# Kernel tuning notes

Measured on AMD Instinct MI355X. Metric: run time of the kernel, lower is better.

Reference implementation:

```python
import jax, jax.numpy as jnp
import numpy as np

NCLASS = 21  # num_classes from init
EPS = 1e-6


def setup_inputs() -> dict:
    key = jax.random.key(0)
    k1, k2 = jax.random.split(key)
    feats = jax.random.normal(k1, (8, 256, 64, 64), dtype=jnp.float32)
    masks = jax.random.randint(k2, (8, 256, 256), 0, NCLASS, dtype=jnp.int32)
    return {"feats": feats, "masks": masks}


def reference(feats, masks):
    # feats: [B, C, h, w] float; masks: [B, H, W] int labels
    B, C, _, _ = feats.shape
    H, W = masks.shape[-2:]
    # F.interpolate(..., mode='bilinear', align_corners=False) == half-pixel bilinear resize
    f = jax.image.resize(feats, (B, C, H, W), method="bilinear")  # [B,C,H,W]
    f_flat = f.reshape(B, C, H * W)  # [B,C,P]

    # labels > nclass (e.g. 255 ignore) are clamped to the dump bucket `nclass`;
    # pixels with label == nclass are excluded (one_hot drops out-of-range rows).
    lbl = jnp.where(masks > NCLASS, NCLASS, masks).reshape(B, H * W)  # [B,P]
    onehot = jax.nn.one_hot(lbl, NCLASS, dtype=f.dtype)  # [B,P,K], dump bucket -> all zeros

    # segment-reduce: per-image per-class feature sums and pixel counts
    sums = jnp.einsum("bcp,bpk->bkc", f_flat, onehot)  # [B,K,C]
    counts = onehot.sum(axis=1)  # [B,K]
    per_img = sums / (counts[..., None] + EPS)  # [B,K,C]; absent classes -> ~0, matching torch loop skip
    prototypes = per_img.mean(axis=0)  # [K,C] (sum over batch / b)
    return prototypes
```

## Files before the change

### kernel.cpp

```cpp
#include <hip/hip_runtime.h>

#define NK 21
#define NC 256
#define NSRC 64
#define NOUT 256
#define NB 8
#define NSL 128
#define NG 8
#define EPS 1e-6f

__device__ __forceinline__ void lds_fadd(float* p, float v) {
  __hip_atomic_fetch_add(p, v, __ATOMIC_RELAXED, __HIP_MEMORY_SCOPE_WORKGROUP);
}

__global__ __launch_bounds__(256, 4)
void proto_main(const float* __restrict__ feats,
                const int* __restrict__ masks,
                float* __restrict__ psum,
                float* __restrict__ pcnt) {
  __shared__ __align__(16) float Wl[NK * 32];
  __shared__ int hist[NK];

  const int tid = threadIdx.x;
  const int r0 = blockIdx.x;
  const int b = blockIdx.y;
  const int z = blockIdx.z;

  const float4* fbase = (const float4*)(
      feats + ((size_t)(b * NC + tid) << 12) + (size_t)r0 * 64 + 32 * z);
  const float4 f0 = fbase[0], f1 = fbase[1], f2 = fbase[2], f3 = fbase[3];
  const float4 f4 = fbase[4], f5 = fbase[5], f6 = fbase[6], f7 = fbase[7];

  for (int i = tid; i < NK * 32; i += 256) Wl[i] = 0.f;
  if (tid < NK) hist[tid] = 0;
  __syncthreads();

  int ylo = 4 * r0 - 2; if (ylo < 0) ylo = 0;
  int yhi = 4 * r0 + 5; if (yhi > NOUT - 1) yhi = NOUT - 1;
  const int xlo = z ? 126 : 0;
  const int npix = (yhi - ylo + 1) * 130;
  const int own_lo = 4 * r0;

  for (int i = tid; i < npix; i += 256) {
    const int x = xlo + i % 130;
    const int y = ylo + i / 130;
    const int lbl = masks[((size_t)b * NOUT + y) * NOUT + x];
    if ((unsigned)lbl < NK) {
      const int ry = y >> 2, py = y & 3;
      const int j0y = (py < 2) ? ry - 1 : ry;
      const float fy = (py == 0) ? 0.625f : (py == 1) ? 0.875f
                     : (py == 2) ? 0.125f : 0.375f;
      const int rx = x >> 2, px = x & 3;
      const int j0x = (px < 2) ? rx - 1 : rx;
      const float fx = (px == 0) ? 0.625f : (px == 1) ? 0.875f
                     : (px == 2) ? 0.125f : 0.375f;

      const int cx0 = (j0x < 0) ? 0 : j0x;
      const int cx1 = (j0x + 1 > NSRC - 1) ? NSRC - 1 : j0x + 1;
      const float wx0 = 1.f - fx, wx1 = fx;
      const int ry0 = (j0y < 0) ? 0 : j0y;
      const int ry1 = (j0y + 1 > NSRC - 1) ? NSRC - 1 : j0y + 1;
      const float wy0 = 1.f - fy, wy1 = fy;

      float* Wk = &Wl[lbl * 32];
      if (ry0 == r0) {
        if ((cx0 >> 5) == z) lds_fadd(&Wk[cx0 & 31], wy0 * wx0);
        if ((cx1 >> 5) == z) lds_fadd(&Wk[cx1 & 31], wy0 * wx1);
      }
      if (ry1 == r0) {
        if ((cx0 >> 5) == z) lds_fadd(&Wk[cx0 & 31], wy1 * wx0);
        if ((cx1 >> 5) == z) lds_fadd(&Wk[cx1 & 31], wy1 * wx1);
      }
      if (y >= own_lo && y < own_lo + 4 && (x >> 7) == z)
        atomicAdd(&hist[lbl], 1);
    }
  }
  __syncthreads();

  float acc[NK];
#pragma unroll
  for (int k = 0; k < NK; ++k) acc[k] = 0.f;

  const float4* wb = (const float4*)Wl;
#pragma unroll
  for (int k = 0; k < NK; ++k) {
    const float4 w0 = wb[k * 8 + 0], w1 = wb[k * 8 + 1];
    const float4 w2 = wb[k * 8 + 2], w3 = wb[k * 8 + 3];
    float a = acc[k];
    a = fmaf(f0.x, w0.x, a); a = fmaf(f0.y, w0.y, a);
    a = fmaf(f0.z, w0.z, a); a = fmaf(f0.w, w0.w, a);
    a = fmaf(f1.x, w1.x, a); a = fmaf(f1.y, w1.y, a);
    a = fmaf(f1.z, w1.z, a); a = fmaf(f1.w, w1.w, a);
    a = fmaf(f2.x, w2.x, a); a = fmaf(f2.y, w2.y, a);
    a = fmaf(f2.z, w2.z, a); a = fmaf(f2.w, w2.w, a);
    a = fmaf(f3.x, w3.x, a); a = fmaf(f3.y, w3.y, a);
    a = fmaf(f3.z, w3.z, a); a = fmaf(f3.w, w3.w, a);
    acc[k] = a;
  }
#pragma unroll
  for (int k = 0; k < NK; ++k) {
    const float4 w4 = wb[k * 8 + 4], w5 = wb[k * 8 + 5];
    const float4 w6 = wb[k * 8 + 6], w7 = wb[k * 8 + 7];
    float a = acc[k];
    a = fmaf(f4.x, w4.x, a); a = fmaf(f4.y, w4.y, a);
    a = fmaf(f4.z, w4.z, a); a = fmaf(f4.w, w4.w, a);
    a = fmaf(f5.x, w5.x, a); a = fmaf(f5.y, w5.y, a);
    a = fmaf(f5.z, w5.z, a); a = fmaf(f5.w, w5.w, a);
    a = fmaf(f6.x, w6.x, a); a = fmaf(f6.y, w6.y, a);
    a = fmaf(f6.z, w6.z, a); a = fmaf(f6.w, w6.w, a);
    a = fmaf(f7.x, w7.x, a); a = fmaf(f7.y, w7.y, a);
    a = fmaf(f7.z, w7.z, a); a = fmaf(f7.w, w7.w, a);
    acc[k] = a;
  }

  const int sl = r0 * 2 + z;
  float* dst = psum + ((size_t)(b * NSL + sl) * NK) * NC + tid;
#pragma unroll
  for (int k = 0; k < NK; ++k) dst[k * NC] = acc[k];
  if (tid < NK) pcnt[(size_t)(b * NSL + sl) * NK + tid] = (float)hist[tid];
}

__global__ __launch_bounds__(256)
void proto_finalA(const float* __restrict__ psum,
                  const float* __restrict__ pcnt,
                  float* __restrict__ psum2,
                  float* __restrict__ pcnt2) {
  const int k = blockIdx.x;
  const int b = blockIdx.y;
  const int g = blockIdx.z;
  const int c = threadIdx.x;
  const int sl0 = g * 16;
  float s = 0.f, cnt = 0.f;
#pragma unroll
  for (int j = 0; j < 16; ++j) {
    s += psum[((size_t)(b * NSL + sl0 + j) * NK + k) * NC + c];
    cnt += pcnt[(size_t)(b * NSL + sl0 + j) * NK + k];
  }
  psum2[((size_t)(b * NG + g) * NK + k) * NC + c] = s;
  if (c == 0) pcnt2[(size_t)(b * NG + g) * NK + k] = cnt;
}

__global__ __launch_bounds__(256)
void proto_finalB(const float* __restrict__ psum2,
                  const float* __restrict__ pcnt2,
                  float* __restrict__ out) {
  const int k = blockIdx.x;
  const int c = threadIdx.x;
  float a = 0.f;
#pragma unroll
  for (int b = 0; b < NB; ++b) {
    float s = 0.f, cnt = 0.f;
#pragma unroll
    for (int g = 0; g < NG; ++g) {
      s += psum2[((size_t)(b * NG + g) * NK + k) * NC + c];
      cnt += pcnt2[(size_t)(b * NG + g) * NK + k];
    }
    a += s / (cnt + EPS);
  }
  out[(size_t)k * NC + c] = a * 0.125f;
}

extern "C" void kernel_launch(void* const* d_in, const int* in_sizes, int n_in,
                              void* d_out, int out_size, void* d_ws, size_t ws_size,
                              hipStream_t stream) {
  const float* feats = (const float*)d_in[0];
  const int* masks = (const int*)d_in[1];
  float* out = (float*)d_out;

  float* psum = (float*)d_ws;
  float* pcnt = psum + (size_t)NB * NSL * NK * NC;
  float* psum2 = pcnt + (size_t)NB * NSL * NK;
  float* pcnt2 = psum2 + (size_t)NB * NG * NK * NC;

  proto_main<<<dim3(64, NB, 2), 256, 0, stream>>>(feats, masks, psum, pcnt);
  proto_finalA<<<dim3(NK, NB, NG), 256, 0, stream>>>(psum, pcnt, psum2, pcnt2);
  proto_finalB<<<dim3(NK), 256, 0, stream>>>(psum2, pcnt2, out);
}
```

Measured before the change: 100.3 us.

## Merge column halves into one block, one pixel column per thread

```diff
diff --git a/kernel.cpp b/kernel.cpp
--- a/kernel.cpp
+++ b/kernel.cpp
@@ -5,7 +5,7 @@
 #define NSRC 64
 #define NOUT 256
 #define NB 8
-#define NSL 128
+#define NSL 64
 #define NG 8
 #define EPS 1e-6f
 
@@ -13,111 +13,121 @@
   __hip_atomic_fetch_add(p, v, __ATOMIC_RELAXED, __HIP_MEMORY_SCOPE_WORKGROUP);
 }
 
-__global__ __launch_bounds__(256, 4)
+__device__ __forceinline__ float d4(float s, float4 a, float4 w) {
+  s = fmaf(a.x, w.x, s); s = fmaf(a.y, w.y, s);
+  s = fmaf(a.z, w.z, s); return fmaf(a.w, w.w, s);
+}
+
+__global__ __launch_bounds__(256, 2)
 void proto_main(const float* __restrict__ feats,
                 const int* __restrict__ masks,
                 float* __restrict__ psum,
                 float* __restrict__ pcnt) {
-  __shared__ __align__(16) float Wl[NK * 32];
+  __shared__ __align__(16) float Wl[NK * 64];
+  __shared__ __align__(16) float Red[NK * NC];
   __shared__ int hist[NK];
 
   const int tid = threadIdx.x;
   const int r0 = blockIdx.x;
-  const int b = blockIdx.y;
-  const int z = blockIdx.z;
+  const int bi = blockIdx.y;
+  const int w = tid >> 6;
+  const int l = tid & 63;
+  const int z = w >> 1;
+  const int c0 = ((w & 1) << 7) | (l << 1);
 
-  const float4* fbase = (const float4*)(
-      feats + ((size_t)(b * NC + tid) << 12) + (size_t)r0 * 64 + 32 * z);
-  const float4 f0 = fbase[0], f1 = fbase[1], f2 = fbase[2], f3 = fbase[3];
-  const float4 f4 = fbase[4], f5 = fbase[5], f6 = fbase[6], f7 = fbase[7];
+  int ylo = 4 * r0 - 2; if (ylo < 0) ylo = 0;
+  int yhi = 4 * r0 + 5; if (yhi > NOUT - 1) yhi = NOUT - 1;
+  const int nr = yhi - ylo + 1;
+  const int x = tid;
+  int lab[8];
+#pragma unroll
+  for (int j = 0; j < 8; ++j)
+    lab[j] = (j < nr) ? masks[((size_t)bi * NOUT + ylo + j) * NOUT + x] : NK;
 
-  for (int i = tid; i < NK * 32; i += 256) Wl[i] = 0.f;
+  const float4* fA = (const float4*)(feats + (((size_t)(bi * NC + c0)) << 12) +
+                                     (size_t)r0 * 64 + 32 * z);
+  const float4* fB = (const float4*)((const float*)fA + 4096);
+  const float4 a0 = fA[0], a1 = fA[1], a2 = fA[2], a3 = fA[3];
+  const float4 a4 = fA[4], a5 = fA[5], a6 = fA[6], a7 = fA[7];
+  const float4 e0 = fB[0], e1 = fB[1], e2 = fB[2], e3 = fB[3];
+  const float4 e4 = fB[4], e5 = fB[5], e6 = fB[6], e7 = fB[7];
+
+  for (int i = tid; i < NK * 64; i += 256) Wl[i] = 0.f;
   if (tid < NK) hist[tid] = 0;
   __syncthreads();
 
-  int ylo = 4 * r0 - 2; if (ylo < 0) ylo = 0;
-  int yhi = 4 * r0 + 5; if (yhi > NOUT - 1) yhi = NOUT - 1;
-  const int xlo = z ? 126 : 0;
-  const int npix = (yhi - ylo + 1) * 130;
-  const int own_lo = 4 * r0;
+  const int rx = x >> 2, px = x & 3;
+  const int j0x = (px < 2) ? rx - 1 : rx;
+  const float fx = (px == 0) ? 0.625f : (px == 1) ? 0.875f
+                 : (px == 2) ? 0.125f : 0.375f;
+  const int cx0 = (j0x < 0) ? 0 : j0x;
+  const int cx1 = (j0x + 1 > NSRC - 1) ? NSRC - 1 : j0x + 1;
+  const float wx0 = 1.f - fx, wx1 = fx;
 
-  for (int i = tid; i < npix; i += 256) {
-    const int x = xlo + i % 130;
-    const int y = ylo + i / 130;
-    const int lbl = masks[((size_t)b * NOUT + y) * NOUT + x];
-    if ((unsigned)lbl < NK) {
-      const int ry = y >> 2, py = y & 3;
-      const int j0y = (py < 2) ? ry - 1 : ry;
-      const float fy = (py == 0) ? 0.625f : (py == 1) ? 0.875f
-                     : (py == 2) ? 0.125f : 0.375f;
-      const int rx = x >> 2, px = x & 3;
-      const int j0x = (px < 2) ? rx - 1 : rx;
-      const float fx = (px == 0) ? 0.625f : (px == 1) ? 0.875f
-                     : (px == 2) ? 0.125f : 0.375f;
-
-      const int cx0 = (j0x < 0) ? 0 : j0x;
-      const int cx1 = (j0x + 1 > NSRC - 1) ? NSRC - 1 : j0x + 1;
-      const float wx0 = 1.f - fx, wx1 = fx;
-      const int ry0 = (j0y < 0) ? 0 : j0y;
-      const int ry1 = (j0y + 1 > NSRC - 1) ? NSRC - 1 : j0y + 1;
-      const float wy0 = 1.f - fy, wy1 = fy;
-
-      float* Wk = &Wl[lbl * 32];
-      if (ry0 == r0) {
-        if ((cx0 >> 5) == z) lds_fadd(&Wk[cx0 & 31], wy0 * wx0);
-        if ((cx1 >> 5) == z) lds_fadd(&Wk[cx1 & 31], wy0 * wx1);
+#pragma unroll
+  for (int j = 0; j < 8; ++j) {
+    if (j < nr) {
+      const int y = ylo + j;
+      const int lbl = lab[j];
+      if ((unsigned)lbl < NK) {
+        const int ry = y >> 2, py = y & 3;
+        const int j0y = (py < 2) ? ry - 1 : ry;
+        const float fy = (py == 0) ? 0.625f : (py == 1) ? 0.875f
+                       : (py == 2) ? 0.125f : 0.375f;
+        const int ry0 = (j0y < 0) ? 0 : j0y;
+        const int ry1 = (j0y + 1 > NSRC - 1) ? NSRC - 1 : j0y + 1;
+        float* Wk = &Wl[lbl << 6];
+        if (ry0 == r0) {
+          lds_fadd(&Wk[cx0], (1.f - fy) * wx0);
+          lds_fadd(&Wk[cx1], (1.f - fy) * wx1);
+        }
+        if (ry1 == r0) {
+          lds_fadd(&Wk[cx0], fy * wx0);
+          lds_fadd(&Wk[cx1], fy * wx1);
+        }
+        if ((unsigned)(y - 4 * r0) < 4u)
+          atomicAdd(&hist[lbl], 1);
       }
-      if (ry1 == r0) {
-        if ((cx0 >> 5) == z) lds_fadd(&Wk[cx0 & 31], wy1 * wx0);
-        if ((cx1 >> 5) == z) lds_fadd(&Wk[cx1 & 31], wy1 * wx1);
-      }
-      if (y >= own_lo && y < own_lo + 4 && (x >> 7) == z)
-        atomicAdd(&hist[lbl], 1);
     }
   }
   __syncthreads();
 
-  float acc[NK];
+  float accA[NK], accB[NK];
 #pragma unroll
-  for (int k = 0; k < NK; ++k) acc[k] = 0.f;
+  for (int k = 0; k < NK; ++k) { accA[k] = 0.f; accB[k] = 0.f; }
 
-  const float4* wb = (const float4*)Wl;
+  const float4* wb = (const float4*)&Wl[z * 32];
 #pragma unroll
   for (int k = 0; k < NK; ++k) {
-    const float4 w0 = wb[k * 8 + 0], w1 = wb[k * 8 + 1];
-    const float4 w2 = wb[k * 8 + 2], w3 = wb[k * 8 + 3];
-    float a = acc[k];
-    a = fmaf(f0.x, w0.x, a); a = fmaf(f0.y, w0.y, a);
-    a = fmaf(f0.z, w0.z, a); a = fmaf(f0.w, w0.w, a);
-    a = fmaf(f1.x, w1.x, a); a = fmaf(f1.y, w1.y, a);
-    a = fmaf(f1.z, w1.z, a); a = fmaf(f1.w, w1.w, a);
-    a = fmaf(f2.x, w2.x, a); a = fmaf(f2.y, w2.y, a);
-    a = fmaf(f2.z, w2.z, a); a = fmaf(f2.w, w2.w, a);
-    a = fmaf(f3.x, w3.x, a); a = fmaf(f3.y, w3.y, a);
-    a = fmaf(f3.z, w3.z, a); a = fmaf(f3.w, w3.w, a);
-    acc[k] = a;
-  }
-#pragma unroll
-  for (int k = 0; k < NK; ++k) {
-    const float4 w4 = wb[k * 8 + 4], w5 = wb[k * 8 + 5];
-    const float4 w6 = wb[k * 8 + 6], w7 = wb[k * 8 + 7];
-    float a = acc[k];
-    a = fmaf(f4.x, w4.x, a); a = fmaf(f4.y, w4.y, a);
-    a = fmaf(f4.z, w4.z, a); a = fmaf(f4.w, w4.w, a);
-    a = fmaf(f5.x, w5.x, a); a = fmaf(f5.y, w5.y, a);
-    a = fmaf(f5.z, w5.z, a); a = fmaf(f5.w, w5.w, a);
-    a = fmaf(f6.x, w6.x, a); a = fmaf(f6.y, w6.y, a);
-    a = fmaf(f6.z, w6.z, a); a = fmaf(f6.w, w6.w, a);
-    a = fmaf(f7.x, w7.x, a); a = fmaf(f7.y, w7.y, a);
-    a = fmaf(f7.z, w7.z, a); a = fmaf(f7.w, w7.w, a);
-    acc[k] = a;
+    const float4 w0 = wb[k * 16 + 0], w1 = wb[k * 16 + 1];
+    const float4 w2 = wb[k * 16 + 2], w3 = wb[k * 16 + 3];
+    const float4 w4 = wb[k * 16 + 4], w5 = wb[k * 16 + 5];
+    const float4 w6 = wb[k * 16 + 6], w7 = wb[k * 16 + 7];
+    float sA = accA[k];
+    sA = d4(sA, a0, w0); sA = d4(sA, a1, w1); sA = d4(sA, a2, w2); sA = d4(sA, a3, w3);
+    sA = d4(sA, a4, w4); sA = d4(sA, a5, w5); sA = d4(sA, a6, w6); sA = d4(sA, a7, w7);
+    accA[k] = sA;
+    float sB = accB[k];
+    sB = d4(sB, e0, w0); sB = d4(sB, e1, w1); sB = d4(sB, e2, w2); sB = d4(sB, e3, w3);
+    sB = d4(sB, e4, w4); sB = d4(sB, e5, w5); sB = d4(sB, e6, w6); sB = d4(sB, e7, w7);
+    accB[k] = sB;
   }
 
-  const int sl = r0 * 2 + z;
-  float* dst = psum + ((size_t)(b * NSL + sl) * NK) * NC + tid;
+  if (w >= 2) {
 #pragma unroll
-  for (int k = 0; k < NK; ++k) dst[k * NC] = acc[k];
-  if (tid < NK) pcnt[(size_t)(b * NSL + sl) * NK + tid] = (float)hist[tid];
+    for (int k = 0; k < NK; ++k)
+      *(float2*)&Red[k * NC + c0] = make_float2(accA[k], accB[k]);
+  }
+  __syncthreads();
+  if (w < 2) {
+    float* dst = psum + ((size_t)(bi * NSL + r0) * NK) * NC + c0;
+#pragma unroll
+    for (int k = 0; k < NK; ++k) {
+      const float2 r = *(const float2*)&Red[k * NC + c0];
+      *(float2*)&dst[k * NC] = make_float2(accA[k] + r.x, accB[k] + r.y);
+    }
+  }
+  if (tid < NK) pcnt[(size_t)(bi * NSL + r0) * NK + tid] = (float)hist[tid];
 }
 
 __global__ __launch_bounds__(256)
@@ -129,10 +139,10 @@
   const int b = blockIdx.y;
   const int g = blockIdx.z;
   const int c = threadIdx.x;
-  const int sl0 = g * 16;
+  const int sl0 = g * (NSL / NG);
   float s = 0.f, cnt = 0.f;
 #pragma unroll
-  for (int j = 0; j < 16; ++j) {
+  for (int j = 0; j < NSL / NG; ++j) {
     s += psum[((size_t)(b * NSL + sl0 + j) * NK + k) * NC + c];
     cnt += pcnt[(size_t)(b * NSL + sl0 + j) * NK + k];
   }
@@ -172,7 +182,7 @@
   float* psum2 = pcnt + (size_t)NB * NSL * NK;
   float* pcnt2 = psum2 + (size_t)NB * NG * NK * NC;
 
-  proto_main<<<dim3(64, NB, 2), 256, 0, stream>>>(feats, masks, psum, pcnt);
+  proto_main<<<dim3(64, NB), 256, 0, stream>>>(feats, masks, psum, pcnt);
   proto_finalA<<<dim3(NK, NB, NG), 256, 0, stream>>>(psum, pcnt, psum2, pcnt2);
   proto_finalB<<<dim3(NK), 256, 0, stream>>>(psum2, pcnt2, out);
 }
```

Measured after the change: 100.5 us. Within noise of the previous version (+0.1%).
